# Performance work log

Measured on AMD Instinct MI355X. Metric: run time of the kernel, lower is better.

The kernel has to match this reference:

```python
import jax, jax.numpy as jnp
import numpy as np

B, S, DM, H, FF = 2, 2048, 1024, 16, 4096
DH = DM // H
EPS = 1e-5


def setup_inputs() -> dict:
    key = jax.random.key(0)
    ks = jax.random.split(key, 16)
    s = 0.02
    return {
        "x": jax.random.normal(ks[0], (B, S, DM), jnp.float32),
        "mask": jnp.ones((B, S), jnp.int32),
        "Wq": jax.random.normal(ks[1], (DM, DM), jnp.float32) * s,
        "bq": jnp.zeros((DM,), jnp.float32),
        "Wk": jax.random.normal(ks[2], (DM, DM), jnp.float32) * s,
        "bk": jnp.zeros((DM,), jnp.float32),
        "Wv": jax.random.normal(ks[3], (DM, DM), jnp.float32) * s,
        "bv": jnp.zeros((DM,), jnp.float32),
        "Wo": jax.random.normal(ks[4], (DM, DM), jnp.float32) * s,
        "bo": jnp.zeros((DM,), jnp.float32),
        "W1": jax.random.normal(ks[5], (DM, FF), jnp.float32) * s,
        "b1": jnp.zeros((FF,), jnp.float32),
        "W2": jax.random.normal(ks[6], (FF, DM), jnp.float32) * s,
        "b2": jnp.zeros((DM,), jnp.float32),
        "g1": jnp.ones((DM,), jnp.float32),
        "beta1": jnp.zeros((DM,), jnp.float32),
        "g2": jnp.ones((DM,), jnp.float32),
        "beta2": jnp.zeros((DM,), jnp.float32),
    }


def _layer_norm(x, g, b):
    mu = jnp.mean(x, axis=-1, keepdims=True)
    var = jnp.var(x, axis=-1, keepdims=True)
    return (x - mu) * jax.lax.rsqrt(var + EPS) * g + b


def reference(x, mask, Wq, bq, Wk, bk, Wv, bv, Wo, bo, W1, b1, W2, b2, g1, beta1, g2, beta2):
    # --- hollow multi-head attention ---
    q = (x @ Wq + bq).reshape(B, S, H, DH)
    k = (x @ Wk + bk).reshape(B, S, H, DH)
    v = (x @ Wv + bv).reshape(B, S, H, DH)
    scores = jnp.einsum("bqhd,bkhd->bhqk", q, k) / jnp.sqrt(jnp.float32(DH))
    # triu(diag=1) and tril(diag=-1) masks kill everything off-diagonal
    diag = jnp.eye(S, dtype=bool)  # [S, S]
    scores = jnp.where(diag[None, None], scores, -jnp.inf)
    attn = jax.nn.softmax(scores, axis=-1)
    out = jnp.einsum("bhqk,bkhd->bqhd", attn, v).reshape(B, S, DM)
    attn_out = out @ Wo + bo
    # --- residual + LN1 ---
    h = _layer_norm(x + attn_out, g1, beta1)
    # --- FFN ---
    ff = jax.nn.relu(h @ W1 + b1) @ W2 + b2
    # --- residual + LN2 ---
    return _layer_norm(h + ff, g2, beta2)
```

## Files before the change

kernel.cpp:

```cpp
#include <hip/hip_runtime.h>
#include <stdint.h>

typedef __bf16 bf16x8 __attribute__((ext_vector_type(8)));
typedef float f32x4 __attribute__((ext_vector_type(4)));

__device__ __forceinline__ uint16_t f2bf(float f) {
  union { float f; uint32_t u; } c; c.f = f;
  uint32_t u = c.u;
  u += 0x7fffu + ((u >> 16) & 1u);
  return (uint16_t)(u >> 16);
}
__device__ __forceinline__ float bf2f(uint16_t u) {
  union { uint32_t u; float f; } c; c.u = (uint32_t)u << 16; return c.f;
}

__global__ void cvt_bf16_kernel(const float* __restrict__ in, uint16_t* __restrict__ out, int n4) {
  int i = blockIdx.x * blockDim.x + threadIdx.x;
  if (i >= n4) return;
  float4 v = reinterpret_cast<const float4*>(in)[i];
  ushort4 o;
  o.x = f2bf(v.x); o.y = f2bf(v.y); o.z = f2bf(v.z); o.w = f2bf(v.w);
  reinterpret_cast<ushort4*>(out)[i] = o;
}

__global__ void transpose_cvt_kernel(const float* __restrict__ in, uint16_t* __restrict__ out,
                                     int R, int C) {
  __shared__ float t[32][33];
  const int tx = threadIdx.x, ty = threadIdx.y;
  const int c0 = blockIdx.x * 32, r0 = blockIdx.y * 32;
#pragma unroll
  for (int i = 0; i < 4; ++i)
    t[ty + i * 8][tx] = in[(size_t)(r0 + ty + i * 8) * C + (c0 + tx)];
  __syncthreads();
#pragma unroll
  for (int i = 0; i < 4; ++i)
    out[(size_t)(c0 + ty + i * 8) * R + (r0 + tx)] = f2bf(t[tx][ty + i * 8]);
}

__global__ void bc_kernel(const float* __restrict__ bv, const float* __restrict__ Wo,
                          const float* __restrict__ bo, float* __restrict__ bc) {
  const int jl = threadIdx.x & 31, kg = threadIdx.x >> 5;
  const int j = blockIdx.x * 32 + jl;
  float s = 0.f;
  const int k0 = kg * 128;
  for (int k = k0; k < k0 + 128; ++k)
    s += bv[k] * Wo[(size_t)k * 1024 + j];
  __shared__ float red[8][32];
  red[kg][jl] = s;
  __syncthreads();
  if (kg == 0) {
    float t = bo[j];
#pragma unroll
    for (int q = 0; q < 8; ++q) t += red[q][jl];
    bc[j] = t;
  }
}

constexpr int BM = 128, BN = 128, BK = 64;

template <int MODE>
__launch_bounds__(256, 2)
__global__ void gemm2ph_kernel(const uint16_t* __restrict__ A, const uint16_t* __restrict__ Bt,
                               const float* __restrict__ bias, const float* __restrict__ res,
                               void* __restrict__ out, int M, int N, int Klen, int lda, int ldb) {
  __shared__ uint16_t sAB[2][2][BM * BK];
  const int tid  = threadIdx.x;
  const int lane = tid & 63;
  const int wave = tid >> 6;

  const int nwg = gridDim.x * gridDim.y;
  int wg = blockIdx.y * gridDim.x + blockIdx.x;
  wg = (wg & 7) * (nwg >> 3) + (wg >> 3);
  const int bx = wg % gridDim.x, by = wg / gridDim.x;
  const int m0 = by * BM, n0 = bx * BN;

  const int z = blockIdx.z;
  A  += (size_t)z * Klen;
  Bt += (size_t)z * Klen;

  const int wm = (wave >> 1) * 64;
  const int wn = (wave & 1) * 64;

  f32x4 acc[4][4] = {};

  const int srow = tid >> 3;
  const int scol = ((tid & 7) ^ (srow & 7)) * 8;
  const uint16_t* ga[4];
  const uint16_t* gb[4];
  uint32_t loff[4];
#pragma unroll
  for (int g = 0; g < 4; ++g) {
    const int row = srow + 32 * g;
    ga[g] = A + (size_t)(m0 + row) * lda + scol;
    gb[g] = Bt + (size_t)(n0 + row) * ldb + scol;
    loff[g] = (uint32_t)(tid + g * 256) * 8;
  }

  const int fr = lane & 15;
  const int hi = lane >> 4;
  const int rx = fr & 7;

  const int nk = Klen / BK;

#define STAGE(buf, kt)                                                                    \
  {                                                                                       \
    _Pragma("unroll")                                                                     \
    for (int g = 0; g < 4; ++g) {                                                         \
      __builtin_amdgcn_global_load_lds(                                                   \
          (const __attribute__((address_space(1))) uint32_t*)(ga[g] + (size_t)(kt) * BK), \
          (__attribute__((address_space(3))) uint32_t*)(&sAB[buf][0][loff[g]]), 16, 0, 0);\
      __builtin_amdgcn_global_load_lds(                                                   \
          (const __attribute__((address_space(1))) uint32_t*)(gb[g] + (size_t)(kt) * BK), \
          (__attribute__((address_space(3))) uint32_t*)(&sAB[buf][1][loff[g]]), 16, 0, 0);\
    }                                                                                     \
  }

  STAGE(0, 0);
  __syncthreads();

  int cur = 0;
  for (int kt = 0; kt < nk; ++kt) {
    if (kt + 1 < nk) STAGE(cur ^ 1, kt + 1);
    const uint16_t* pA = &sAB[cur][0][0];
    const uint16_t* pB = &sAB[cur][1][0];
    bf16x8 af[4][2], bb[4][2];
#pragma unroll
    for (int m = 0; m < 4; ++m)
#pragma unroll
      for (int ks = 0; ks < 2; ++ks) {
        const int slot = (ks * 4 + hi) ^ rx;
        af[m][ks] = *reinterpret_cast<const bf16x8*>(pA + (wm + m * 16 + fr) * BK + slot * 8);
        bb[m][ks] = *reinterpret_cast<const bf16x8*>(pB + (wn + m * 16 + fr) * BK + slot * 8);
      }
#pragma unroll
    for (int ks = 0; ks < 2; ++ks)
#pragma unroll
      for (int m = 0; m < 4; ++m)
#pragma unroll
        for (int n = 0; n < 4; ++n)
          acc[m][n] = __builtin_amdgcn_mfma_f32_16x16x32_bf16(af[m][ks], bb[n][ks], acc[m][n], 0, 0, 0);
    __syncthreads();
    cur ^= 1;
  }
#undef STAGE

  const int cn  = lane & 15;
  const int cm4 = (lane >> 4) * 4;
  float* outf = (MODE == 3) ? ((float*)out + (size_t)z * M * N) : (float*)out;
#pragma unroll
  for (int m = 0; m < 4; ++m) {
#pragma unroll
    for (int n = 0; n < 4; ++n) {
      const int gm = m0 + wm + m * 16 + cm4;
      const int gn = n0 + wn + n * 16 + cn;
      const float bbv = (MODE == 3) ? 0.f : (bias ? bias[gn] : 0.f);
#pragma unroll
      for (int r = 0; r < 4; ++r) {
        const size_t idx = (size_t)(gm + r) * N + gn;
        const float vv = acc[m][n][r] + bbv;
        if constexpr (MODE == 0) {
          ((uint16_t*)out)[idx] = f2bf(vv);
        } else if constexpr (MODE == 1) {
          ((float*)out)[idx] = vv + res[idx];
        } else if constexpr (MODE == 2) {
          ((uint16_t*)out)[idx] = f2bf(fmaxf(vv, 0.f));
        } else {
          outf[idx] = vv;
        }
      }
    }
  }
}

__global__ void ln1_kernel(const float* __restrict__ in,
                           const float* __restrict__ g,
                           const float* __restrict__ b,
                           uint16_t* __restrict__ outb) {
  const int row = blockIdx.x;
  const int t = threadIdx.x;
  const float4 v = reinterpret_cast<const float4*>(in + (size_t)row * 1024)[t];
  float s  = v.x + v.y + v.z + v.w;
  float s2 = v.x * v.x + v.y * v.y + v.z * v.z + v.w * v.w;
#pragma unroll
  for (int o = 32; o > 0; o >>= 1) { s += __shfl_down(s, o); s2 += __shfl_down(s2, o); }
  __shared__ float red[8];
  const int lane = t & 63, wave = t >> 6;
  if (lane == 0) { red[wave] = s; red[4 + wave] = s2; }
  __syncthreads();
  const float S  = red[0] + red[1] + red[2] + red[3];
  const float S2 = red[4] + red[5] + red[6] + red[7];
  const float mu  = S * (1.f / 1024.f);
  const float var = S2 * (1.f / 1024.f) - mu * mu;
  const float rs  = rsqrtf(var + 1e-5f);
  const float4 gg = reinterpret_cast<const float4*>(g)[t];
  const float4 bb = reinterpret_cast<const float4*>(b)[t];
  ushort4 ob;
  ob.x = f2bf((v.x - mu) * rs * gg.x + bb.x);
  ob.y = f2bf((v.y - mu) * rs * gg.y + bb.y);
  ob.z = f2bf((v.z - mu) * rs * gg.z + bb.z);
  ob.w = f2bf((v.w - mu) * rs * gg.w + bb.w);
  reinterpret_cast<ushort4*>(outb + (size_t)row * 1024)[t] = ob;
}

__global__ void ln2_kernel(const float* __restrict__ p0, const float* __restrict__ p1,
                           const uint16_t* __restrict__ hb, const float* __restrict__ b2,
                           const float* __restrict__ g, const float* __restrict__ be,
                           float* __restrict__ out) {
  const int row = blockIdx.x;
  const int t = threadIdx.x;
  const size_t base = (size_t)row * 1024;
  const float4 a = reinterpret_cast<const float4*>(p0 + base)[t];
  const float4 b = reinterpret_cast<const float4*>(p1 + base)[t];
  const ushort4 h4 = reinterpret_cast<const ushort4*>(hb + base)[t];
  const float4 c2 = reinterpret_cast<const float4*>(b2)[t];
  float4 v;
  v.x = a.x + b.x + c2.x + bf2f(h4.x);
  v.y = a.y + b.y + c2.y + bf2f(h4.y);
  v.z = a.z + b.z + c2.z + bf2f(h4.z);
  v.w = a.w + b.w + c2.w + bf2f(h4.w);
  float s  = v.x + v.y + v.z + v.w;
  float s2 = v.x * v.x + v.y * v.y + v.z * v.z + v.w * v.w;
#pragma unroll
  for (int o = 32; o > 0; o >>= 1) { s += __shfl_down(s, o); s2 += __shfl_down(s2, o); }
  __shared__ float red[8];
  const int lane = t & 63, wave = t >> 6;
  if (lane == 0) { red[wave] = s; red[4 + wave] = s2; }
  __syncthreads();
  const float S  = red[0] + red[1] + red[2] + red[3];
  const float S2 = red[4] + red[5] + red[6] + red[7];
  const float mu  = S * (1.f / 1024.f);
  const float var = S2 * (1.f / 1024.f) - mu * mu;
  const float rs  = rsqrtf(var + 1e-5f);
  const float4 gg = reinterpret_cast<const float4*>(g)[t];
  const float4 bb = reinterpret_cast<const float4*>(be)[t];
  float4 o;
  o.x = (v.x - mu) * rs * gg.x + bb.x;
  o.y = (v.y - mu) * rs * gg.y + bb.y;
  o.z = (v.z - mu) * rs * gg.z + bb.z;
  o.w = (v.w - mu) * rs * gg.w + bb.w;
  reinterpret_cast<float4*>(out + base)[t] = o;
}

extern "C" void kernel_launch(void* const* d_in, const int* in_sizes, int n_in,
                              void* d_out, int out_size, void* d_ws, size_t ws_size,
                              hipStream_t stream) {
  const float* x   = (const float*)d_in[0];
  const float* Wv  = (const float*)d_in[6];
  const float* bv  = (const float*)d_in[7];
  const float* Wo  = (const float*)d_in[8];
  const float* bo  = (const float*)d_in[9];
  const float* W1  = (const float*)d_in[10];
  const float* b1  = (const float*)d_in[11];
  const float* W2  = (const float*)d_in[12];
  const float* b2  = (const float*)d_in[13];
  const float* g1  = (const float*)d_in[14];
  const float* be1 = (const float*)d_in[15];
  const float* g2  = (const float*)d_in[16];
  const float* be2 = (const float*)d_in[17];
  float* out = (float*)d_out;

  constexpr int M = 4096, DM = 1024, FF = 4096;

  char* p = (char*)d_ws;
  auto alloc = [&](size_t bytes) {
    char* r = p;
    p += (bytes + 255) & ~(size_t)255;
    return r;
  };
  uint16_t* xb  = (uint16_t*)alloc((size_t)M * DM * 2);
  uint16_t* wvb = (uint16_t*)alloc((size_t)DM * DM * 2);
  uint16_t* woT = (uint16_t*)alloc((size_t)DM * DM * 2);
  uint16_t* w1t = (uint16_t*)alloc((size_t)FF * DM * 2);
  uint16_t* w2t = (uint16_t*)alloc((size_t)DM * FF * 2);
  uint16_t* wcT = (uint16_t*)alloc((size_t)DM * DM * 2);
  float*    bc  = (float*)   alloc((size_t)DM * 4);
  float*    r1  = (float*)   alloc((size_t)M * DM * 4);
  uint16_t* hb  = (uint16_t*)alloc((size_t)M * DM * 2);
  uint16_t* tb  = (uint16_t*)alloc((size_t)M * FF * 2);
  float*    pp  = (float*)   alloc((size_t)2 * M * DM * 4);

  const dim3 tb32(32, 8);

  cvt_bf16_kernel<<<M * DM / 4 / 256, 256, 0, stream>>>(x, xb, M * DM / 4);
  cvt_bf16_kernel<<<DM * DM / 4 / 256, 256, 0, stream>>>(Wv, wvb, DM * DM / 4);
  transpose_cvt_kernel<<<dim3(DM / 32, DM / 32), tb32, 0, stream>>>(Wo, woT, DM, DM);
  transpose_cvt_kernel<<<dim3(FF / 32, DM / 32), tb32, 0, stream>>>(W1, w1t, DM, FF);
  transpose_cvt_kernel<<<dim3(DM / 32, FF / 32), tb32, 0, stream>>>(W2, w2t, FF, DM);
  bc_kernel<<<32, 256, 0, stream>>>(bv, Wo, bo, bc);

  gemm2ph_kernel<0><<<dim3(DM / BN, DM / BM), 256, 0, stream>>>(
      woT, wvb, nullptr, nullptr, wcT, DM, DM, DM, DM, DM);
  gemm2ph_kernel<1><<<dim3(DM / BN, M / BM), 256, 0, stream>>>(
      xb, wcT, bc, x, r1, M, DM, DM, DM, DM);
  ln1_kernel<<<M, 256, 0, stream>>>(r1, g1, be1, hb);
  gemm2ph_kernel<2><<<dim3(FF / BN, M / BM), 256, 0, stream>>>(
      hb, w1t, b1, nullptr, tb, M, FF, DM, DM, DM);
  gemm2ph_kernel<3><<<dim3(DM / BN, M / BM, 2), 256, 0, stream>>>(
      tb, w2t, nullptr, nullptr, pp, M, DM, FF / 2, FF, FF);
  ln2_kernel<<<M, 256, 0, stream>>>(pp, pp + (size_t)M * DM, hb, b2, g2, be2, out);
}
```

Baseline: 162.8 us.

## Add 256x256 eight-wave GEMM kernel for FFN with split-K=4 and bf16 partials

Adds a new 512-thread GEMM kernel with 256x256 tiles, 128KB dynamic LDS, a finer-grained staged prefetch of quarter-tiles, and MFMA priority hints. It is used for both FFN GEMMs. The second FFN GEMM changes from split-K 2 with fp32 partials to split-K 4 with bf16 partials, and LN2 sums the four partials. The aim is more operand reuse per tile and better load/compute overlap, at the cost of lower occupancy, fewer workgroups on the W1 GEMM, and bf16 rounding of the partial sums.

New measurement: 162.0 us. Within noise of the previous version (-0.5%).

```diff
diff --git a/kernel.cpp b/kernel.cpp
--- a/kernel.cpp
+++ b/kernel.cpp
@@ -74,10 +74,6 @@
   const int bx = wg % gridDim.x, by = wg / gridDim.x;
   const int m0 = by * BM, n0 = bx * BN;
 
-  const int z = blockIdx.z;
-  A  += (size_t)z * Klen;
-  Bt += (size_t)z * Klen;
-
   const int wm = (wave >> 1) * 64;
   const int wn = (wave & 1) * 64;
 
@@ -102,7 +98,7 @@
 
   const int nk = Klen / BK;
 
-#define STAGE(buf, kt)                                                                    \
+#define STAGE2(buf, kt)                                                                   \
   {                                                                                       \
     _Pragma("unroll")                                                                     \
     for (int g = 0; g < 4; ++g) {                                                         \
@@ -115,12 +111,12 @@
     }                                                                                     \
   }
 
-  STAGE(0, 0);
+  STAGE2(0, 0);
   __syncthreads();
 
   int cur = 0;
   for (int kt = 0; kt < nk; ++kt) {
-    if (kt + 1 < nk) STAGE(cur ^ 1, kt + 1);
+    if (kt + 1 < nk) STAGE2(cur ^ 1, kt + 1);
     const uint16_t* pA = &sAB[cur][0][0];
     const uint16_t* pB = &sAB[cur][1][0];
     bf16x8 af[4][2], bb[4][2];
@@ -142,30 +138,161 @@
     __syncthreads();
     cur ^= 1;
   }
-#undef STAGE
+#undef STAGE2
 
   const int cn  = lane & 15;
   const int cm4 = (lane >> 4) * 4;
-  float* outf = (MODE == 3) ? ((float*)out + (size_t)z * M * N) : (float*)out;
 #pragma unroll
   for (int m = 0; m < 4; ++m) {
 #pragma unroll
     for (int n = 0; n < 4; ++n) {
       const int gm = m0 + wm + m * 16 + cm4;
       const int gn = n0 + wn + n * 16 + cn;
-      const float bbv = (MODE == 3) ? 0.f : (bias ? bias[gn] : 0.f);
+      const float bbv = bias ? bias[gn] : 0.f;
 #pragma unroll
       for (int r = 0; r < 4; ++r) {
         const size_t idx = (size_t)(gm + r) * N + gn;
         const float vv = acc[m][n][r] + bbv;
         if constexpr (MODE == 0) {
           ((uint16_t*)out)[idx] = f2bf(vv);
-        } else if constexpr (MODE == 1) {
+        } else {
           ((float*)out)[idx] = vv + res[idx];
-        } else if constexpr (MODE == 2) {
-          ((uint16_t*)out)[idx] = f2bf(fmaxf(vv, 0.f));
+        }
+      }
+    }
+  }
+}
+
+template <int MODE>
+__launch_bounds__(512, 2)
+__global__ void gemm8ph_kernel(const uint16_t* __restrict__ A, const uint16_t* __restrict__ Bt,
+                               const float* __restrict__ bias, void* __restrict__ out,
+                               int M, int N, int Klen, int lda, int ldb) {
+  extern __shared__ uint16_t lds[];
+  const int tid  = threadIdx.x;
+  const int lane = tid & 63;
+  const int wave = tid >> 6;
+
+  const int nwg = gridDim.x * gridDim.y;
+  int wg = blockIdx.y * gridDim.x + blockIdx.x;
+  wg = (wg & 7) * (nwg >> 3) + (wg >> 3);
+  const int bx = wg % gridDim.x, by = wg / gridDim.x;
+  const int m0 = by * 256, n0 = bx * 256;
+
+  const int z = blockIdx.z;
+  A  += (size_t)z * Klen;
+  Bt += (size_t)z * Klen;
+
+  const int wm = (wave >> 2) * 128;
+  const int wn = (wave & 3) * 64;
+
+  f32x4 acc[8][4] = {};
+
+  const int R0 = tid >> 2;
+  const int sg = ((tid & 3) ^ (((tid >> 2) ^ (tid >> 4)) & 3)) * 8;
+  const uint16_t* gA0 = A + (size_t)(m0 + R0) * lda + sg;
+  const uint16_t* gA1 = A + (size_t)(m0 + R0 + 128) * lda + sg;
+  const uint16_t* gB0 = Bt + (size_t)(n0 + R0) * ldb + sg;
+  const uint16_t* gB1 = Bt + (size_t)(n0 + R0 + 128) * ldb + sg;
+
+  const int nk = Klen / 64;
+
+#define STAGE8(T, R)                                                                        \
+  if ((T) < nk) {                                                                           \
+    const uint16_t* s0 = (((R) & 1) ? gA0 : gB0) + (size_t)(T) * 64 + ((R) >> 1) * 32;      \
+    const uint16_t* s1 = (((R) & 1) ? gA1 : gB1) + (size_t)(T) * 64 + ((R) >> 1) * 32;      \
+    uint16_t* d = lds + (((T) & 1) * 32768 + (R) * 8192);                                   \
+    __builtin_amdgcn_global_load_lds(                                                       \
+        (const __attribute__((address_space(1))) uint32_t*)s0,                              \
+        (__attribute__((address_space(3))) uint32_t*)(d + (size_t)tid * 8), 16, 0, 0);      \
+    __builtin_amdgcn_global_load_lds(                                                       \
+        (const __attribute__((address_space(1))) uint32_t*)s1,                              \
+        (__attribute__((address_space(3))) uint32_t*)(d + (size_t)(tid + 512) * 8), 16, 0, 0); \
+  }
+
+  const int fr = lane & 15;
+  const int hi = lane >> 4;
+  const int g  = (fr ^ (fr >> 2)) & 3;
+  const int laneA = wm * 32 + fr * 32 + ((hi ^ g) * 8);
+  const int laneB = wn * 32 + fr * 32 + ((hi ^ g) * 8);
+
+  STAGE8(0, 0); STAGE8(0, 1); STAGE8(0, 2); STAGE8(0, 3);
+  asm volatile("s_waitcnt vmcnt(4)" ::: "memory");
+  STAGE8(1, 0); STAGE8(1, 1); STAGE8(1, 2);
+  asm volatile("s_waitcnt vmcnt(6)" ::: "memory");
+  __builtin_amdgcn_s_barrier();
+
+#define MFMA16(MB)                                                        \
+  __builtin_amdgcn_s_setprio(1);                                          \
+  _Pragma("unroll") for (int m = 0; m < 4; ++m)                           \
+    _Pragma("unroll") for (int n = 0; n < 4; ++n)                         \
+      acc[m + (MB)][n] = __builtin_amdgcn_mfma_f32_16x16x32_bf16(         \
+          aq[m], bq[n], acc[m + (MB)][n], 0, 0, 0);                       \
+  __builtin_amdgcn_s_setprio(0);
+
+  for (int k = 0; k < nk; ++k) {
+    const uint16_t* bufp = lds + (k & 1) * 32768;
+    bf16x8 aq[4], bq[4];
+#pragma unroll
+    for (int n = 0; n < 4; ++n) bq[n] = *reinterpret_cast<const bf16x8*>(bufp + 0 * 8192 + laneB + n * 512);
+#pragma unroll
+    for (int m = 0; m < 4; ++m) aq[m] = *reinterpret_cast<const bf16x8*>(bufp + 1 * 8192 + laneA + m * 512);
+    STAGE8(k + 1, 3);
+    __builtin_amdgcn_s_barrier();
+    asm volatile("s_waitcnt lgkmcnt(0)" ::: "memory");
+    MFMA16(0);
+    __builtin_amdgcn_s_barrier();
+#pragma unroll
+    for (int m = 0; m < 4; ++m) aq[m] = *reinterpret_cast<const bf16x8*>(bufp + 1 * 8192 + laneA + (m + 4) * 512);
+    STAGE8(k + 2, 0);
+    __builtin_amdgcn_s_barrier();
+    asm volatile("s_waitcnt lgkmcnt(0)" ::: "memory");
+    MFMA16(4);
+    __builtin_amdgcn_s_barrier();
+#pragma unroll
+    for (int n = 0; n < 4; ++n) bq[n] = *reinterpret_cast<const bf16x8*>(bufp + 2 * 8192 + laneB + n * 512);
+#pragma unroll
+    for (int m = 0; m < 4; ++m) aq[m] = *reinterpret_cast<const bf16x8*>(bufp + 3 * 8192 + laneA + m * 512);
+    STAGE8(k + 2, 1);
+    __builtin_amdgcn_s_barrier();
+    asm volatile("s_waitcnt lgkmcnt(0)" ::: "memory");
+    MFMA16(0);
+    __builtin_amdgcn_s_barrier();
+#pragma unroll
+    for (int m = 0; m < 4; ++m) aq[m] = *reinterpret_cast<const bf16x8*>(bufp + 3 * 8192 + laneA + (m + 4) * 512);
+    STAGE8(k + 2, 2);
+    if (k < nk - 2) { asm volatile("s_waitcnt vmcnt(6)" ::: "memory"); }
+    else            { asm volatile("s_waitcnt vmcnt(0)" ::: "memory"); }
+    __builtin_amdgcn_s_barrier();
+    asm volatile("s_waitcnt lgkmcnt(0)" ::: "memory");
+    MFMA16(4);
+    __builtin_amdgcn_s_barrier();
+  }
+#undef MFMA16
+#undef STAGE8
+
+  const int cn  = lane & 15;
+  const int cm4 = (lane >> 4) * 4;
+  uint16_t* outp = (uint16_t*)out;
+  if constexpr (MODE == 1) outp += (size_t)z * M * N;
+  float bias_n[4];
+  if constexpr (MODE == 0) {
+#pragma unroll
+    for (int n = 0; n < 4; ++n) bias_n[n] = bias[n0 + wn + n * 16 + cn];
+  }
+#pragma unroll
+  for (int m = 0; m < 8; ++m) {
+#pragma unroll
+    for (int n = 0; n < 4; ++n) {
+      const int gm = m0 + wm + m * 16 + cm4;
+      const int gn = n0 + wn + n * 16 + cn;
+#pragma unroll
+      for (int r = 0; r < 4; ++r) {
+        const size_t idx = (size_t)(gm + r) * N + gn;
+        if constexpr (MODE == 0) {
+          outp[idx] = f2bf(fmaxf(acc[m][n][r] + bias_n[n], 0.f));
         } else {
-          outf[idx] = vv;
+          outp[idx] = f2bf(acc[m][n][r]);
         }
       }
     }
@@ -202,22 +329,23 @@
   reinterpret_cast<ushort4*>(outb + (size_t)row * 1024)[t] = ob;
 }
 
-__global__ void ln2_kernel(const float* __restrict__ p0, const float* __restrict__ p1,
+__global__ void ln2_kernel(const uint16_t* __restrict__ pp, size_t pstride,
                            const uint16_t* __restrict__ hb, const float* __restrict__ b2,
                            const float* __restrict__ g, const float* __restrict__ be,
                            float* __restrict__ out) {
   const int row = blockIdx.x;
   const int t = threadIdx.x;
   const size_t base = (size_t)row * 1024;
-  const float4 a = reinterpret_cast<const float4*>(p0 + base)[t];
-  const float4 b = reinterpret_cast<const float4*>(p1 + base)[t];
   const ushort4 h4 = reinterpret_cast<const ushort4*>(hb + base)[t];
   const float4 c2 = reinterpret_cast<const float4*>(b2)[t];
   float4 v;
-  v.x = a.x + b.x + c2.x + bf2f(h4.x);
-  v.y = a.y + b.y + c2.y + bf2f(h4.y);
-  v.z = a.z + b.z + c2.z + bf2f(h4.z);
-  v.w = a.w + b.w + c2.w + bf2f(h4.w);
+  v.x = c2.x + bf2f(h4.x); v.y = c2.y + bf2f(h4.y);
+  v.z = c2.z + bf2f(h4.z); v.w = c2.w + bf2f(h4.w);
+#pragma unroll
+  for (int zz = 0; zz < 4; ++zz) {
+    const ushort4 p4 = reinterpret_cast<const ushort4*>(pp + zz * pstride + base)[t];
+    v.x += bf2f(p4.x); v.y += bf2f(p4.y); v.z += bf2f(p4.z); v.w += bf2f(p4.w);
+  }
   float s  = v.x + v.y + v.z + v.w;
   float s2 = v.x * v.x + v.y * v.y + v.z * v.z + v.w * v.w;
 #pragma unroll
@@ -277,7 +405,12 @@
   float*    r1  = (float*)   alloc((size_t)M * DM * 4);
   uint16_t* hb  = (uint16_t*)alloc((size_t)M * DM * 2);
   uint16_t* tb  = (uint16_t*)alloc((size_t)M * FF * 2);
-  float*    pp  = (float*)   alloc((size_t)2 * M * DM * 4);
+  uint16_t* pp  = (uint16_t*)alloc((size_t)4 * M * DM * 2);
+
+  (void)hipFuncSetAttribute(reinterpret_cast<const void*>(gemm8ph_kernel<0>),
+                            hipFuncAttributeMaxDynamicSharedMemorySize, 131072);
+  (void)hipFuncSetAttribute(reinterpret_cast<const void*>(gemm8ph_kernel<1>),
+                            hipFuncAttributeMaxDynamicSharedMemorySize, 131072);
 
   const dim3 tb32(32, 8);
 
@@ -293,9 +426,9 @@
   gemm2ph_kernel<1><<<dim3(DM / BN, M / BM), 256, 0, stream>>>(
       xb, wcT, bc, x, r1, M, DM, DM, DM, DM);
   ln1_kernel<<<M, 256, 0, stream>>>(r1, g1, be1, hb);
-  gemm2ph_kernel<2><<<dim3(FF / BN, M / BM), 256, 0, stream>>>(
-      hb, w1t, b1, nullptr, tb, M, FF, DM, DM, DM);
-  gemm2ph_kernel<3><<<dim3(DM / BN, M / BM, 2), 256, 0, stream>>>(
-      tb, w2t, nullptr, nullptr, pp, M, DM, FF / 2, FF, FF);
-  ln2_kernel<<<M, 256, 0, stream>>>(pp, pp + (size_t)M * DM, hb, b2, g2, be2, out);
-}
+  gemm8ph_kernel<0><<<dim3(FF / 256, M / 256), 512, 131072, stream>>>(
+      hb, w1t, b1, tb, M, FF, DM, DM, DM);
+  gemm8ph_kernel<1><<<dim3(DM / 256, M / 256, 4), 512, 131072, stream>>>(
+      tb, w2t, nullptr, pp, M, DM, FF / 4, FF, FF);
+  ln2_kernel<<<M, 256, 0, stream>>>(pp, (size_t)M * DM, hb, b2, g2, be2, out);
+}
```
